# Optimization experiments

Measured on AMD Instinct MI355X. Metric: run time of the kernel, lower is better.

The kernel has to match this reference:

```python
import jax, jax.numpy as jnp
import numpy as np

D = 512
H = 8
DK = D // H
EXP = 2
EPS = 1e-5


def _layernorm(x, g, b):
    mu = jnp.mean(x, axis=-1, keepdims=True)
    var = jnp.mean(jnp.square(x - mu), axis=-1, keepdims=True)
    return (x - mu) * jax.lax.rsqrt(var + EPS) * g + b


def setup_inputs() -> dict:
    key = jax.random.key(0)
    ks = jax.random.split(key, 10)
    B, C = 4, 2048
    s = 0.02
    return {
        "h": jax.random.normal(ks[0], (B, C, D), jnp.float32),
        "adj_bias": jax.random.normal(ks[1], (B, C, C), jnp.float32),
        "w_qkv": jax.random.normal(ks[2], (D, 3 * D), jnp.float32) * s,
        "b_qkv": jnp.zeros((3 * D,), jnp.float32),
        "w_out": jax.random.normal(ks[3], (D, D), jnp.float32) * s,
        "b_out": jnp.zeros((D,), jnp.float32),
        "ln1_g": jnp.ones((D,), jnp.float32),
        "ln1_b": jnp.zeros((D,), jnp.float32),
        "ln2_g": jnp.ones((D,), jnp.float32),
        "ln2_b": jnp.zeros((D,), jnp.float32),
        "w1": jax.random.normal(ks[4], (D, D * EXP), jnp.float32) * s,
        "b1": jnp.zeros((D * EXP,), jnp.float32),
        "w2": jax.random.normal(ks[5], (D * EXP, D), jnp.float32) * s,
        "b2": jnp.zeros((D,), jnp.float32),
    }


def reference(h, adj_bias, w_qkv, b_qkv, w_out, b_out, ln1_g, ln1_b, ln2_g, ln2_b, w1, b1, w2, b2):
    B, C, _ = h.shape
    scale = DK ** -0.5
    h_n = _layernorm(h, ln1_g, ln1_b)
    qkv = (h_n @ w_qkv + b_qkv).reshape(B, C, 3, H, DK)
    q, k, v = (qkv[:, :, i].transpose(0, 2, 1, 3) for i in range(3))  # (B,H,C,DK)
    logits = jnp.einsum('bhqd,bhkd->bhqk', q, k) * scale + adj_bias[:, None, :, :]
    attn = jax.nn.softmax(logits, axis=-1)  # (B,H,C,C); dropout off (eval)
    out = jnp.einsum('bhqk,bhkd->bhqd', attn, v).transpose(0, 2, 1, 3).reshape(B, C, D)
    h = h + out @ w_out + b_out
    ff = _layernorm(h, ln2_g, ln2_b)
    ff = jax.nn.gelu(ff @ w1 + b1, approximate=False) @ w2 + b2
    return h + ff
```

## Files before the change

kernel.cpp:

```cpp
#include <hip/hip_runtime.h>
#include <hip/hip_bf16.h>

#define BDIM 4
#define CDIM 2048
#define DDIM 512
#define HH   8
#define DKH  64
#define NROW (BDIM * CDIM)

typedef unsigned short u16;
typedef unsigned int   u32;
typedef u16   u16x4  __attribute__((ext_vector_type(4)));
typedef u16   u16x8  __attribute__((ext_vector_type(8)));
typedef u32   u32x4  __attribute__((ext_vector_type(4)));
typedef __bf16 bf16x8 __attribute__((ext_vector_type(8)));
typedef __bf16 bf16x2 __attribute__((ext_vector_type(2)));
typedef float f32x4  __attribute__((ext_vector_type(4)));
typedef float f32x16 __attribute__((ext_vector_type(16)));

#define LOG2E 1.4426950408889634f

__device__ __forceinline__ u16 f2bf(float f) {
  union { float f; unsigned u; } x; x.f = f;
  unsigned u = x.u;
  u += 0x7fffu + ((u >> 16) & 1u);
  return (u16)(u >> 16);
}
__device__ __forceinline__ float bf2f(u16 u) {
  return __builtin_bit_cast(float, (u32)u << 16);
}
__device__ __forceinline__ u32 pk2(float a, float b) {
  bf16x2 t; t[0] = (__bf16)a; t[1] = (__bf16)b;
  return __builtin_bit_cast(u32, t);
}

__device__ __forceinline__ void gload_lds16(const u16* gp, u16* lp) {
  __builtin_amdgcn_global_load_lds((__attribute__((address_space(1))) const void*)gp,
                                   (__attribute__((address_space(3))) void*)lp, 16, 0, 0);
}

__global__ __launch_bounds__(256) void ln_kernel(const float* __restrict__ x,
                                                 const float* __restrict__ gamma,
                                                 const float* __restrict__ beta,
                                                 u16* __restrict__ y, int nrows) {
  int gw = (blockIdx.x * 256 + threadIdx.x) >> 6;
  int l  = threadIdx.x & 63;
  if (gw >= nrows) return;
  const float* xr = x + (size_t)gw * DDIM;
  float4 a = *(const float4*)(xr + l * 8);
  float4 b = *(const float4*)(xr + l * 8 + 4);
  float s = a.x + a.y + a.z + a.w + b.x + b.y + b.z + b.w;
  float q = a.x*a.x + a.y*a.y + a.z*a.z + a.w*a.w + b.x*b.x + b.y*b.y + b.z*b.z + b.w*b.w;
#pragma unroll
  for (int m = 1; m < 64; m <<= 1) { s += __shfl_xor(s, m); q += __shfl_xor(q, m); }
  float mu  = s * (1.0f / DDIM);
  float var = q * (1.0f / DDIM) - mu * mu;
  float rs  = rsqrtf(var + 1e-5f);
  float4 g0 = *(const float4*)(gamma + l * 8);
  float4 g1 = *(const float4*)(gamma + l * 8 + 4);
  float4 b0 = *(const float4*)(beta + l * 8);
  float4 b1 = *(const float4*)(beta + l * 8 + 4);
  u16x8 o;
  o[0] = f2bf((a.x - mu) * rs * g0.x + b0.x);
  o[1] = f2bf((a.y - mu) * rs * g0.y + b0.y);
  o[2] = f2bf((a.z - mu) * rs * g0.z + b0.z);
  o[3] = f2bf((a.w - mu) * rs * g0.w + b0.w);
  o[4] = f2bf((b.x - mu) * rs * g1.x + b1.x);
  o[5] = f2bf((b.y - mu) * rs * g1.y + b1.y);
  o[6] = f2bf((b.z - mu) * rs * g1.z + b1.z);
  o[7] = f2bf((b.w - mu) * rs * g1.w + b1.w);
  *(u16x8*)(y + (size_t)gw * DDIM + l * 8) = o;
}

__global__ __launch_bounds__(256) void transpose_w(const float* __restrict__ w,
                                                   u16* __restrict__ wt, int K, int N) {
  int idx = blockIdx.x * 256 + threadIdx.x;
  int kb  = K >> 3;
  if (idx >= N * kb) return;
  int n = idx / kb, k0 = (idx - n * kb) * 8;
  u16x8 o;
#pragma unroll
  for (int j = 0; j < 8; ++j) o[j] = f2bf(w[(size_t)(k0 + j) * N + n]);
  *(u16x8*)(wt + (size_t)n * K + k0) = o;
}

__global__ __launch_bounds__(256) void adj_transform(const float* __restrict__ adj,
                                                     u16* __restrict__ adjC) {
  const int bkt = blockIdx.y;
  const int b = bkt >> 5, kt = bkt & 31;
  const int q0 = blockIdx.x * 256;
  const int t = threadIdx.x;
  const int ch = t & 7, c16 = ch & 3, hi2 = ch >> 2, m = c16 >> 1;
  const int K0 = m * 32 + ((c16 * 2) & 3) * 8 + hi2 * 4;
#pragma unroll
  for (int itq = 0; itq < 8; ++itq) {
    int q = q0 + itq * 32 + (t >> 3);
    const float* src = adj + ((size_t)b * CDIM + q) * CDIM + kt * 64;
    f32x4 v0 = *(const f32x4*)(src + K0);
    f32x4 v1 = *(const f32x4*)(src + K0 + 8);
    u16x8 o;
    o[0] = f2bf(v0[0] * LOG2E); o[1] = f2bf(v0[1] * LOG2E);
    o[2] = f2bf(v0[2] * LOG2E); o[3] = f2bf(v0[3] * LOG2E);
    o[4] = f2bf(v1[0] * LOG2E); o[5] = f2bf(v1[1] * LOG2E);
    o[6] = f2bf(v1[2] * LOG2E); o[7] = f2bf(v1[3] * LOG2E);
    *(u16x8*)(adjC + ((size_t)(b * 32 + kt) * 2048 + q) * 64 + ch * 8) = o;
  }
}

template <int EPI>
__global__ __launch_bounds__(256) void gemm128(const u16* __restrict__ A,
                                               const u16* __restrict__ Bt,
                                               const float* __restrict__ bias,
                                               const float* __restrict__ res,
                                               float* __restrict__ outf,
                                               u16* __restrict__ outb,
                                               u16* __restrict__ outq,
                                               u16* __restrict__ outk,
                                               u16* __restrict__ outv,
                                               int M, int N, int K) {
  __shared__ u16 As[2][128 * 32];
  __shared__ u16 Bs[2][128 * 32];
  const int tid = threadIdx.x;
  const int w = tid >> 6, l = tid & 63;
  const int l15 = l & 15, l4 = l >> 4;
  const int bm = blockIdx.y, bn = blockIdx.x;
  const int wr = w >> 1, wc = w & 1;

  f32x4 acc[4][4] = {};

  const u16* Ag = A  + (size_t)(bm * 128 + w * 32 + (l >> 2)) * K + (l & 3) * 8;
  const u16* Bg = Bt + (size_t)(bn * 128 + w * 32 + (l >> 2)) * K + (l & 3) * 8;

  auto stage = [&](int buf, int k0) {
    gload_lds16(Ag + k0, &As[buf][(w * 2 + 0) * 512]);
    gload_lds16(Ag + (size_t)16 * K + k0, &As[buf][(w * 2 + 1) * 512]);
    gload_lds16(Bg + k0, &Bs[buf][(w * 2 + 0) * 512]);
    gload_lds16(Bg + (size_t)16 * K + k0, &Bs[buf][(w * 2 + 1) * 512]);
  };

  stage(0, 0);
  __syncthreads();
  int cur = 0;
  for (int k0 = 0; k0 < K; k0 += 32) {
    if (k0 + 32 < K) stage(cur ^ 1, k0 + 32);
    bf16x8 af[4], bf[4];
#pragma unroll
    for (int m = 0; m < 4; ++m)
      af[m] = *(const bf16x8*)(&As[cur][(wr * 64 + m * 16 + l15) * 32 + l4 * 8]);
#pragma unroll
    for (int n = 0; n < 4; ++n)
      bf[n] = *(const bf16x8*)(&Bs[cur][(wc * 64 + n * 16 + l15) * 32 + l4 * 8]);
#pragma unroll
    for (int m = 0; m < 4; ++m)
#pragma unroll
      for (int n = 0; n < 4; ++n)
        acc[m][n] = __builtin_amdgcn_mfma_f32_16x16x32_bf16(af[m], bf[n], acc[m][n], 0, 0, 0);
    __syncthreads();
    cur ^= 1;
  }

#pragma unroll
  for (int m = 0; m < 4; ++m) {
    const int row0 = bm * 128 + wr * 64 + m * 16 + l4 * 4;
#pragma unroll
    for (int n = 0; n < 4; ++n) {
      const int col = bn * 128 + wc * 64 + n * 16 + l15;
      const float bv = bias[col];
#pragma unroll
      for (int r = 0; r < 4; ++r) {
        const int row = row0 + r;
        float val = acc[m][n][r] + bv;
        if constexpr (EPI == 0) {
          int t = col >> 9, hh = (col >> 6) & 7, dk = col & 63;
          int bb = row >> 11, cc = row & 2047;
          if (t == 0) {
            val *= 0.125f * LOG2E;
            outq[(((size_t)bb * HH + hh) * CDIM + cc) * DKH + dk] = f2bf(val);
          } else if (t == 1) {
            outk[(((size_t)bb * HH + hh) * CDIM + cc) * DKH + dk] = f2bf(val);
          } else {
            outv[(((size_t)bb * HH + hh) * DKH + dk) * CDIM + cc] = f2bf(val);
          }
        } else if constexpr (EPI == 1) {
          size_t idx = (size_t)row * N + col;
          outf[idx] = val + res[idx];
        } else {
          float g = 0.5f * val * (1.0f + erff(val * 0.70710678118f));
          outb[(size_t)row * N + col] = f2bf(g);
        }
      }
    }
  }
}

__global__ __launch_bounds__(512, 2) void flash_attn(const u16* __restrict__ Q,
                                                     const u16* __restrict__ Kg,
                                                     const u16* __restrict__ Vt,
                                                     const u16* __restrict__ adjC,
                                                     u16* __restrict__ O) {
  __shared__ u16 Ks[2][2][64 * 64];
  __shared__ u16 Vs[2][2][64 * 64];
  __shared__ float lw[4][32];
  __shared__ float lsx[4][32];
  const int flat = blockIdx.x + 16 * blockIdx.y;
  const int virt = (flat & 7) * 64 + (flat >> 3);
  const int qt = virt & 15;
  const int bh = virt >> 4;
  const int b = bh >> 3, hh = bh & 7;
  const int tid = threadIdx.x;
  const int w = tid >> 6, l = tid & 63;
  const int kh = w >> 2, qg = w & 3;
  const int q32 = l & 31, hi = l >> 5;
  const int qglob = qt * 128 + qg * 32 + q32;

  const u16* Qb = Q  + (size_t)bh * CDIM * DKH;
  const u16* Kb = Kg + (size_t)bh * CDIM * DKH;
  const u16* Vb = Vt + (size_t)bh * DKH * CDIM;

  const int srow = qg * 16 + (l >> 3);
  const int sg   = (l & 7) ^ (l >> 3);
  const u16* Kg0 = Kb + (size_t)(srow + 0) * DKH + sg * 8;
  const u16* Kg1 = Kb + (size_t)(srow + 8) * DKH + sg * 8;
  const u16* Vg0 = Vb + (size_t)(srow + 0) * CDIM + sg * 8;
  const u16* Vg1 = Vb + (size_t)(srow + 8) * CDIM + sg * 8;

  bf16x8 qf[4];
#pragma unroll
  for (int s = 0; s < 4; ++s)
    qf[s] = *(const bf16x8*)(Qb + (size_t)qglob * DKH + s * 16 + hi * 8);

  const u16* adjQ = adjC + ((size_t)(b * 32) * 2048 + qglob) * 64 + hi * 32;

  f32x16 oa[2] = {};
  float lsum = 0.f;

  auto stage = [&](int buf, int ktr) {
    int kta = kh * 16 + ktr;
    gload_lds16(Kg0 + (size_t)kta * 4096, &Ks[kh][buf][(qg * 16 + 0) * 64]);
    gload_lds16(Kg1 + (size_t)kta * 4096, &Ks[kh][buf][(qg * 16 + 8) * 64]);
    gload_lds16(Vg0 + kta * 64, &Vs[kh][buf][(qg * 16 + 0) * 64]);
    gload_lds16(Vg1 + kta * 64, &Vs[kh][buf][(qg * 16 + 8) * 64]);
  };
  auto ajload = [&](u16x8* dst, int ktr) {
    const u16* p = adjQ + (size_t)(kh * 16 + ktr) * 131072;
#pragma unroll
    for (int i = 0; i < 4; ++i) dst[i] = *(const u16x8*)(p + i * 8);
  };
  auto computeQK = [&](const u16* KsB, const u16x8* av, f32x16* sa) {
#pragma unroll
    for (int m = 0; m < 2; ++m)
#pragma unroll
      for (int r = 0; r < 16; ++r)
        sa[m][r] = bf2f(av[m * 2 + (r >> 3)][r & 7]);
    __builtin_amdgcn_s_setprio(1);
#pragma unroll
    for (int s = 0; s < 4; ++s)
#pragma unroll
      for (int m = 0; m < 2; ++m) {
        bf16x8 kf = *(const bf16x8*)(&KsB[(m * 32 + q32) * 64 + (((s * 2 + hi) ^ (q32 & 7)) * 8)]);
        sa[m] = __builtin_amdgcn_mfma_f32_32x32x16_bf16(kf, qf[s], sa[m], 0, 0, 0);
      }
    __builtin_amdgcn_s_setprio(0);
  };
  auto computePV = [&](const u16* VsB, f32x16* sa) {
#pragma unroll
    for (int m = 0; m < 2; ++m)
#pragma unroll
      for (int r = 0; r < 16; ++r) {
        float p = exp2f(sa[m][r]);
        sa[m][r] = p;
        lsum += p;
      }
    bf16x8 af[4];
#pragma unroll
    for (int m = 0; m < 2; ++m)
#pragma unroll
      for (int t2 = 0; t2 < 2; ++t2) {
        u32 w0 = pk2(sa[m][t2 * 8 + 0], sa[m][t2 * 8 + 1]);
        u32 w1 = pk2(sa[m][t2 * 8 + 2], sa[m][t2 * 8 + 3]);
        u32 w2 = pk2(sa[m][t2 * 8 + 4], sa[m][t2 * 8 + 5]);
        u32 w3 = pk2(sa[m][t2 * 8 + 6], sa[m][t2 * 8 + 7]);
        u32 pw0 = (u32)__shfl_xor((int)w0, 32);
        u32 pw1 = (u32)__shfl_xor((int)w1, 32);
        u32 pw2 = (u32)__shfl_xor((int)w2, 32);
        u32 pw3 = (u32)__shfl_xor((int)w3, 32);
        u32x4 aw;
        aw[0] = hi ? pw2 : w0;
        aw[1] = hi ? pw3 : w1;
        aw[2] = hi ? w2 : pw0;
        aw[3] = hi ? w3 : pw1;
        af[m * 2 + t2] = __builtin_bit_cast(bf16x8, aw);
      }
    __builtin_amdgcn_s_setprio(1);
#pragma unroll
    for (int s = 0; s < 4; ++s)
#pragma unroll
      for (int n = 0; n < 2; ++n) {
        bf16x8 vf = *(const bf16x8*)(&VsB[(n * 32 + q32) * 64 + (((s * 2 + hi) ^ (q32 & 7)) * 8)]);
        oa[n] = __builtin_amdgcn_mfma_f32_32x32x16_bf16(af[s], vf, oa[n], 0, 0, 0);
      }
    __builtin_amdgcn_s_setprio(0);
  };

  u16x8 avA[4], avB[4];
  f32x16 sa[2];
  stage(0, 0);
  ajload(avA, 0);
  __syncthreads();
#pragma unroll 1
  for (int it = 0; it < 8; ++it) {
    int ktr = it * 2;
    stage(1, ktr + 1);
    computeQK(&Ks[kh][0][0], avA, sa);
    ajload(avB, ktr + 1);
    computePV(&Vs[kh][0][0], sa);
    __syncthreads();
    if (ktr + 2 < 16) stage(0, ktr + 2);
    computeQK(&Ks[kh][1][0], avB, sa);
    if (ktr + 2 < 16) ajload(avA, ktr + 2);
    computePV(&Vs[kh][1][0], sa);
    __syncthreads();
  }

  lsum += __shfl_xor(lsum, 32);

  float* cb = (float*)&Vs[0][0][0];
  if (kh == 1) {
#pragma unroll
    for (int n = 0; n < 2; ++n)
#pragma unroll
      for (int r = 0; r < 16; ++r)
        cb[((qg * 2 + n) * 16 + r) * 64 + l] = oa[n][r];
    if (hi == 0) lsx[qg][q32] = lsum;
  }
  __syncthreads();
  if (kh == 0) {
    lsum += lsx[qg][q32];
#pragma unroll
    for (int n = 0; n < 2; ++n)
#pragma unroll
      for (int r = 0; r < 16; ++r)
        oa[n][r] += cb[((qg * 2 + n) * 16 + r) * 64 + l];
    lw[qg][q32] = 1.0f / lsum;
#pragma unroll
    for (int n = 0; n < 2; ++n)
#pragma unroll
      for (int r = 0; r < 16; ++r) {
        int qloc = (r & 3) + 8 * (r >> 2) + 4 * hi;
        int row = qt * 128 + qg * 32 + qloc;
        float val = oa[n][r] * lw[qg][qloc];
        O[((size_t)b * CDIM + row) * DDIM + hh * 64 + n * 32 + q32] = f2bf(val);
      }
  }
}

extern "C" void kernel_launch(void* const* d_in, const int* in_sizes, int n_in,
                              void* d_out, int out_size, void* d_ws, size_t ws_size,
                              hipStream_t stream) {
  const float* h      = (const float*)d_in[0];
  const float* adj    = (const float*)d_in[1];
  const float* w_qkv  = (const float*)d_in[2];
  const float* b_qkv  = (const float*)d_in[3];
  const float* w_out  = (const float*)d_in[4];
  const float* b_out  = (const float*)d_in[5];
  const float* ln1g   = (const float*)d_in[6];
  const float* ln1b   = (const float*)d_in[7];
  const float* ln2g   = (const float*)d_in[8];
  const float* ln2b   = (const float*)d_in[9];
  const float* w1     = (const float*)d_in[10];
  const float* b1     = (const float*)d_in[11];
  const float* w2     = (const float*)d_in[12];
  const float* b2     = (const float*)d_in[13];
  float* out = (float*)d_out;

  char* ws = (char*)d_ws;
  u16* adjC  = (u16*)(ws);
  u16* hn    = (u16*)(ws + 33554432);
  u16* qb    = (u16*)(ws + 41943040);
  u16* kb    = (u16*)(ws + 50331648);
  u16* vt    = (u16*)(ws + 58720256);
  u16* attn  = (u16*)(ws + 67108864);
  u16* wqkvt = (u16*)(ws + 75497472);
  u16* woutt = (u16*)(ws + 77070336);
  u16* w1t   = (u16*)(ws + 77594624);
  u16* w2t   = (u16*)(ws + 78643200);
  u16* ffin  = hn;
  u16* ffmid = qb;

  adj_transform<<<dim3(8, 128), 256, 0, stream>>>(adj, adjC);

  transpose_w<<<384, 256, 0, stream>>>(w_qkv, wqkvt, 512, 1536);
  transpose_w<<<128, 256, 0, stream>>>(w_out, woutt, 512, 512);
  transpose_w<<<256, 256, 0, stream>>>(w1, w1t, 512, 1024);
  transpose_w<<<256, 256, 0, stream>>>(w2, w2t, 1024, 512);

  ln_kernel<<<2048, 256, 0, stream>>>(h, ln1g, ln1b, hn, NROW);

  gemm128<0><<<dim3(12, 64), 256, 0, stream>>>(hn, wqkvt, b_qkv, nullptr,
                                               nullptr, nullptr, qb, kb, vt,
                                               NROW, 3 * DDIM, DDIM);

  flash_attn<<<dim3(16, 32), 512, 0, stream>>>(qb, kb, vt, adjC, attn);

  gemm128<1><<<dim3(4, 64), 256, 0, stream>>>(attn, woutt, b_out, h,
                                              out, nullptr, nullptr, nullptr, nullptr,
                                              NROW, DDIM, DDIM);

  ln_kernel<<<2048, 256, 0, stream>>>(out, ln2g, ln2b, ffin, NROW);

  gemm128<2><<<dim3(8, 64), 256, 0, stream>>>(ffin, w1t, b1, nullptr,
                                              nullptr, ffmid, nullptr, nullptr, nullptr,
                                              NROW, 2 * DDIM, DDIM);

  gemm128<1><<<dim3(4, 64), 256, 0, stream>>>(ffmid, w2t, b2, out,
                                              out, nullptr, nullptr, nullptr, nullptr,
                                              NROW, DDIM, 2 * DDIM);
}
```

Baseline: 217.4 us.

## Shrink GEMM M-tile to 64, merge weight transposes, use raw exp and permlane swap

The GEMM block tile drops from 128x128 to 64x128, so each wave computes a 64x32 strip and the grids double in M. This raises block count for the small N GEMMs at the cost of less A/B reuse per block. The four weight-transpose launches become one kernel, removing launch overhead. In attention, exp2f is replaced by a raw v_exp_f32 instruction, and the xor-32 shuffles plus selects become permlane32_swap to cut cross-lane traffic.

```diff
diff --git a/kernel.cpp b/kernel.cpp
--- a/kernel.cpp
+++ b/kernel.cpp
@@ -32,6 +32,11 @@
 __device__ __forceinline__ u32 pk2(float a, float b) {
   bf16x2 t; t[0] = (__bf16)a; t[1] = (__bf16)b;
   return __builtin_bit_cast(u32, t);
+}
+__device__ __forceinline__ float fexp2(float x) {
+  float r;
+  asm("v_exp_f32 %0, %1" : "=v"(r) : "v"(x));
+  return r;
 }
 
 __device__ __forceinline__ void gload_lds16(const u16* gp, u16* lp) {
@@ -72,11 +77,21 @@
   *(u16x8*)(y + (size_t)gw * DDIM + l * 8) = o;
 }
 
-__global__ __launch_bounds__(256) void transpose_w(const float* __restrict__ w,
-                                                   u16* __restrict__ wt, int K, int N) {
+__global__ __launch_bounds__(256) void transpose_all(const float* __restrict__ wqkv,
+                                                     const float* __restrict__ wout,
+                                                     const float* __restrict__ w1,
+                                                     const float* __restrict__ w2,
+                                                     u16* __restrict__ o_qkv,
+                                                     u16* __restrict__ o_out,
+                                                     u16* __restrict__ o_w1,
+                                                     u16* __restrict__ o_w2) {
   int idx = blockIdx.x * 256 + threadIdx.x;
-  int kb  = K >> 3;
-  if (idx >= N * kb) return;
+  const float* w; u16* wt; int K, N;
+  if (idx < 98304)       { w = wqkv; wt = o_qkv; K = 512;  N = 1536; }
+  else if (idx < 131072) { idx -= 98304;  w = wout; wt = o_out; K = 512;  N = 512; }
+  else if (idx < 196608) { idx -= 131072; w = w1;   wt = o_w1;  K = 512;  N = 1024; }
+  else                   { idx -= 196608; w = w2;   wt = o_w2;  K = 1024; N = 512; }
+  int kb = K >> 3;
   int n = idx / kb, k0 = (idx - n * kb) * 8;
   u16x8 o;
 #pragma unroll
@@ -108,34 +123,32 @@
 }
 
 template <int EPI>
-__global__ __launch_bounds__(256) void gemm128(const u16* __restrict__ A,
-                                               const u16* __restrict__ Bt,
-                                               const float* __restrict__ bias,
-                                               const float* __restrict__ res,
-                                               float* __restrict__ outf,
-                                               u16* __restrict__ outb,
-                                               u16* __restrict__ outq,
-                                               u16* __restrict__ outk,
-                                               u16* __restrict__ outv,
-                                               int M, int N, int K) {
-  __shared__ u16 As[2][128 * 32];
+__global__ __launch_bounds__(256) void gemm64(const u16* __restrict__ A,
+                                              const u16* __restrict__ Bt,
+                                              const float* __restrict__ bias,
+                                              const float* __restrict__ res,
+                                              float* __restrict__ outf,
+                                              u16* __restrict__ outb,
+                                              u16* __restrict__ outq,
+                                              u16* __restrict__ outk,
+                                              u16* __restrict__ outv,
+                                              int M, int N, int K) {
+  __shared__ u16 As[2][64 * 32];
   __shared__ u16 Bs[2][128 * 32];
   const int tid = threadIdx.x;
   const int w = tid >> 6, l = tid & 63;
   const int l15 = l & 15, l4 = l >> 4;
   const int bm = blockIdx.y, bn = blockIdx.x;
-  const int wr = w >> 1, wc = w & 1;
-
-  f32x4 acc[4][4] = {};
-
-  const u16* Ag = A  + (size_t)(bm * 128 + w * 32 + (l >> 2)) * K + (l & 3) * 8;
+
+  f32x4 acc[4][2] = {};
+
+  const u16* Ag = A  + (size_t)(bm * 64 + w * 16 + (l >> 2)) * K + (l & 3) * 8;
   const u16* Bg = Bt + (size_t)(bn * 128 + w * 32 + (l >> 2)) * K + (l & 3) * 8;
 
   auto stage = [&](int buf, int k0) {
-    gload_lds16(Ag + k0, &As[buf][(w * 2 + 0) * 512]);
-    gload_lds16(Ag + (size_t)16 * K + k0, &As[buf][(w * 2 + 1) * 512]);
-    gload_lds16(Bg + k0, &Bs[buf][(w * 2 + 0) * 512]);
-    gload_lds16(Bg + (size_t)16 * K + k0, &Bs[buf][(w * 2 + 1) * 512]);
+    gload_lds16(Ag + k0, &As[buf][w * 512]);
+    gload_lds16(Bg + k0, &Bs[buf][w * 1024]);
+    gload_lds16(Bg + (size_t)16 * K + k0, &Bs[buf][w * 1024 + 512]);
   };
 
   stage(0, 0);
@@ -143,17 +156,17 @@
   int cur = 0;
   for (int k0 = 0; k0 < K; k0 += 32) {
     if (k0 + 32 < K) stage(cur ^ 1, k0 + 32);
-    bf16x8 af[4], bf[4];
+    bf16x8 af[4], bf[2];
 #pragma unroll
     for (int m = 0; m < 4; ++m)
-      af[m] = *(const bf16x8*)(&As[cur][(wr * 64 + m * 16 + l15) * 32 + l4 * 8]);
-#pragma unroll
-    for (int n = 0; n < 4; ++n)
-      bf[n] = *(const bf16x8*)(&Bs[cur][(wc * 64 + n * 16 + l15) * 32 + l4 * 8]);
+      af[m] = *(const bf16x8*)(&As[cur][(m * 16 + l15) * 32 + l4 * 8]);
+#pragma unroll
+    for (int n = 0; n < 2; ++n)
+      bf[n] = *(const bf16x8*)(&Bs[cur][(w * 32 + n * 16 + l15) * 32 + l4 * 8]);
 #pragma unroll
     for (int m = 0; m < 4; ++m)
 #pragma unroll
-      for (int n = 0; n < 4; ++n)
+      for (int n = 0; n < 2; ++n)
         acc[m][n] = __builtin_amdgcn_mfma_f32_16x16x32_bf16(af[m], bf[n], acc[m][n], 0, 0, 0);
     __syncthreads();
     cur ^= 1;
@@ -161,10 +174,10 @@
 
 #pragma unroll
   for (int m = 0; m < 4; ++m) {
-    const int row0 = bm * 128 + wr * 64 + m * 16 + l4 * 4;
-#pragma unroll
-    for (int n = 0; n < 4; ++n) {
-      const int col = bn * 128 + wc * 64 + n * 16 + l15;
+    const int row0 = bm * 64 + m * 16 + l4 * 4;
+#pragma unroll
+    for (int n = 0; n < 2; ++n) {
+      const int col = bn * 128 + w * 32 + n * 16 + l15;
       const float bv = bias[col];
 #pragma unroll
       for (int r = 0; r < 4; ++r) {
@@ -267,7 +280,7 @@
     for (int m = 0; m < 2; ++m)
 #pragma unroll
       for (int r = 0; r < 16; ++r) {
-        float p = exp2f(sa[m][r]);
+        float p = fexp2(sa[m][r]);
         sa[m][r] = p;
         lsum += p;
       }
@@ -280,15 +293,13 @@
         u32 w1 = pk2(sa[m][t2 * 8 + 2], sa[m][t2 * 8 + 3]);
         u32 w2 = pk2(sa[m][t2 * 8 + 4], sa[m][t2 * 8 + 5]);
         u32 w3 = pk2(sa[m][t2 * 8 + 6], sa[m][t2 * 8 + 7]);
-        u32 pw0 = (u32)__shfl_xor((int)w0, 32);
-        u32 pw1 = (u32)__shfl_xor((int)w1, 32);
-        u32 pw2 = (u32)__shfl_xor((int)w2, 32);
-        u32 pw3 = (u32)__shfl_xor((int)w3, 32);
+        auto r02 = __builtin_amdgcn_permlane32_swap(w0, w2, false, false);
+        auto r13 = __builtin_amdgcn_permlane32_swap(w1, w3, false, false);
         u32x4 aw;
-        aw[0] = hi ? pw2 : w0;
-        aw[1] = hi ? pw3 : w1;
-        aw[2] = hi ? w2 : pw0;
-        aw[3] = hi ? w3 : pw1;
+        aw[0] = r02[0];
+        aw[1] = r13[0];
+        aw[2] = r02[1];
+        aw[3] = r13[1];
         af[m * 2 + t2] = __builtin_bit_cast(bf16x8, aw);
       }
     __builtin_amdgcn_s_setprio(1);
@@ -389,30 +400,28 @@
 
   adj_transform<<<dim3(8, 128), 256, 0, stream>>>(adj, adjC);
 
-  transpose_w<<<384, 256, 0, stream>>>(w_qkv, wqkvt, 512, 1536);
-  transpose_w<<<128, 256, 0, stream>>>(w_out, woutt, 512, 512);
-  transpose_w<<<256, 256, 0, stream>>>(w1, w1t, 512, 1024);
-  transpose_w<<<256, 256, 0, stream>>>(w2, w2t, 1024, 512);
+  transpose_all<<<1024, 256, 0, stream>>>(w_qkv, w_out, w1, w2,
+                                          wqkvt, woutt, w1t, w2t);
 
   ln_kernel<<<2048, 256, 0, stream>>>(h, ln1g, ln1b, hn, NROW);
 
-  gemm128<0><<<dim3(12, 64), 256, 0, stream>>>(hn, wqkvt, b_qkv, nullptr,
+  gemm64<0><<<dim3(12, 128), 256, 0, stream>>>(hn, wqkvt, b_qkv, nullptr,
                                                nullptr, nullptr, qb, kb, vt,
                                                NROW, 3 * DDIM, DDIM);
 
   flash_attn<<<dim3(16, 32), 512, 0, stream>>>(qb, kb, vt, adjC, attn);
 
-  gemm128<1><<<dim3(4, 64), 256, 0, stream>>>(attn, woutt, b_out, h,
+  gemm64<1><<<dim3(4, 128), 256, 0, stream>>>(attn, woutt, b_out, h,
                                               out, nullptr, nullptr, nullptr, nullptr,
                                               NROW, DDIM, DDIM);
 
   ln_kernel<<<2048, 256, 0, stream>>>(out, ln2g, ln2b, ffin, NROW);
 
-  gemm128<2><<<dim3(8, 64), 256, 0, stream>>>(ffin, w1t, b1, nullptr,
+  gemm64<2><<<dim3(8, 128), 256, 0, stream>>>(ffin, w1t, b1, nullptr,
                                               nullptr, ffmid, nullptr, nullptr, nullptr,
                                               NROW, 2 * DDIM, DDIM);
 
-  gemm128<1><<<dim3(4, 64), 256, 0, stream>>>(ffmid, w2t, b2, out,
+  gemm64<1><<<dim3(4, 128), 256, 0, stream>>>(ffmid, w2t, b2, out,
                                               out, nullptr, nullptr, nullptr, nullptr,
                                               NROW, DDIM, 2 * DDIM);
 }
```

Measured after the change: 197.1 us. -9.3%, faster.
